# Optimization experiments

Hardware: AMD Instinct MI355X
Metric: run time of the kernel (lower is better)

## Reference

```python
import jax, jax.numpy as jnp
import numpy as np

HEADS = 16
LN_EPS = 1e-5


def setup_inputs() -> dict:
    key = jax.random.key(0)
    ks = jax.random.split(key, 4)
    B, S, C, U = 2, 2048, 1024, 1024
    scale = 1.0 / np.sqrt(C)
    return {
        "inputs": jax.random.normal(ks[0], (B, S, C), dtype=jnp.float32),
        "Wq": jax.random.normal(ks[1], (C, U), dtype=jnp.float32) * scale,
        "bq": jnp.zeros((U,), dtype=jnp.float32),
        "Wk": jax.random.normal(ks[2], (C, U), dtype=jnp.float32) * scale,
        "bk": jnp.zeros((U,), dtype=jnp.float32),
        "Wv": jax.random.normal(ks[3], (C, U), dtype=jnp.float32) * scale,
        "bv": jnp.zeros((U,), dtype=jnp.float32),
        "ln_gamma": jnp.ones((S, U), dtype=jnp.float32),
        "ln_beta": jnp.zeros((S, U), dtype=jnp.float32),
    }


def reference(inputs, Wq, bq, Wk, bk, Wv, bv, ln_gamma, ln_beta):
    B, S, C = inputs.shape
    U = Wq.shape[1]
    H = HEADS
    dh = U // H

    Q = inputs @ Wq + bq  # [B,S,U]
    K = inputs @ Wk + bk
    V = inputs @ Wv + bv

    # torch: concat(split(X, U//H, dim=-1), dim=0) -> head-major stacking on batch
    def split_heads(X):
        return jnp.moveaxis(X.reshape(B, S, H, dh), 2, 0).reshape(H * B, S, dh)

    Q_, K_, V_ = split_heads(Q), split_heads(K), split_heads(V)

    scores = jnp.einsum('bqd,bkd->bqk', Q_, K_) / jnp.sqrt(jnp.float32(dh))
    tri = jnp.tril(jnp.ones((S, S), dtype=bool))  # causal mask
    scores = jnp.where(tri[None, :, :], scores, jnp.float32(-1e9))
    attn = jax.nn.softmax(scores, axis=-1)
    out_ = jnp.einsum('bqk,bkd->bqd', attn, V_)  # [H*B,S,dh]

    # inverse: split on batch into H chunks of size B, concat on feature dim
    out = jnp.moveaxis(out_.reshape(H, B, S, dh), 0, 2).reshape(B, S, U)

    out = out + inputs  # residual

    # LayerNorm over normalized_shape=[S, U] (joint seq+feature stats)
    mu = jnp.mean(out, axis=(-2, -1), keepdims=True)
    var = jnp.mean(jnp.square(out - mu), axis=(-2, -1), keepdims=True)
    out = (out - mu) / jnp.sqrt(var + LN_EPS) * ln_gamma + ln_beta
    return out
```

## Files before the change

kernel.cpp:

```cpp
#include <hip/hip_runtime.h>
#include <hip/hip_bf16.h>


typedef __bf16 bf16_t;
typedef __bf16 bf16x8 __attribute__((ext_vector_type(8)));
typedef __bf16 bf16x4 __attribute__((ext_vector_type(4)));
typedef _Float16 f16_t;
typedef _Float16 f16x2 __attribute__((ext_vector_type(2)));
typedef _Float16 f16x4 __attribute__((ext_vector_type(4)));
typedef _Float16 f16x8 __attribute__((ext_vector_type(8)));
typedef float f32x4 __attribute__((ext_vector_type(4)));

constexpr int Bsz = 2;
constexpr int Seq = 2048;
constexpr int Cdim = 1024;
constexpr int Udim = 1024;
constexpr int Hn = 16;
constexpr int Dh = 64;
constexpr int Mrows = Bsz * Seq;
constexpr int PerBatch = Seq * Udim;
constexpr float SCLQ = 0.125f * 1.44269504088896340736f;

#if __has_builtin(__builtin_amdgcn_exp2f)
#define EXP2F(x) __builtin_amdgcn_exp2f(x)
#else
#define EXP2F(x) exp2f(x)
#endif

#define AINL __attribute__((always_inline))

__device__ __forceinline__ void gload16(const void* g, void* l)
{
    __builtin_amdgcn_global_load_lds(
        (const __attribute__((address_space(1))) void*)g,
        (__attribute__((address_space(3))) void*)l, 16, 0, 0);
}

__device__ __forceinline__ f16x2 pkrtz(float a, float b)
{
    return __builtin_bit_cast(f16x2, __builtin_amdgcn_cvt_pkrtz(a, b));
}

__global__ __launch_bounds__(256)
void prep(const float* __restrict__ X,
          const float* __restrict__ Wq, const float* __restrict__ Wk,
          const float* __restrict__ Wv,
          bf16_t* __restrict__ Xb,
          bf16_t* __restrict__ Tq, bf16_t* __restrict__ Tk,
          bf16_t* __restrict__ Tv, float* __restrict__ stats)
{
    int z = blockIdx.z;
    int tid = threadIdx.x;
    if (z < 3) {
        const float* W = (z == 0) ? Wq : (z == 1) ? Wk : Wv;
        bf16_t* T = (z == 0) ? Tq : (z == 1) ? Tk : Tv;
        __shared__ bf16_t t[64][65];
        int x0 = blockIdx.x * 64, y0 = blockIdx.y * 64;
        int tx = tid & 63, ty = tid >> 6;
        for (int i = ty; i < 64; i += 4)
            t[i][tx] = (bf16_t)W[(size_t)(y0 + i) * Cdim + x0 + tx];
        __syncthreads();
        for (int i = ty; i < 64; i += 4)
            T[(size_t)(x0 + i) * Cdim + y0 + tx] = t[tx][i];
    } else {
        int bi = blockIdx.y * 16 + blockIdx.x;
        if (bi == 0 && tid < 4) stats[tid] = 0.0f;
        const float4* Xv = (const float4*)X;
#pragma unroll
        for (int k = 0; k < 16; k++) {
            int i = bi * 4096 + k * 256 + tid;
            float4 v = Xv[i];
            bf16x4 o = { (bf16_t)v.x, (bf16_t)v.y, (bf16_t)v.z, (bf16_t)v.w };
            *(bf16x4*)(Xb + (size_t)i * 4) = o;
        }
    }
}

__global__ __launch_bounds__(256)
void gemm_qkv(const bf16_t* __restrict__ X,
              const bf16_t* __restrict__ Wt0, const bf16_t* __restrict__ Wt1,
              const bf16_t* __restrict__ Wt2,
              const float* __restrict__ b0, const float* __restrict__ b1,
              const float* __restrict__ b2,
              f16_t* __restrict__ O0, f16_t* __restrict__ O1, f16_t* __restrict__ O2v)
{
    int z = blockIdx.z;
    const bf16_t* Wt = (z == 0) ? Wt0 : (z == 1) ? Wt1 : Wt2;
    const float* bias = (z == 0) ? b0 : (z == 1) ? b1 : b2;
    float scl = (z == 0) ? SCLQ : 1.0f;

    constexpr int Kd = 1024, Nd = 1024;
    __shared__ __align__(16) bf16_t As[128 * 32];
    __shared__ __align__(16) bf16_t Bs[128 * 32];

    int tid = threadIdx.x;
    int wave = tid >> 6, lane = tid & 63, quad = lane >> 4, l16 = lane & 15;
    int wm = (wave & 1) * 64, wn = (wave >> 1) * 64;
    int m0 = blockIdx.y * 128, n0 = blockIdx.x * 128;

    f32x4 acc[4][4] = {};

    int e0 = wave * 512 + lane * 8;
    int r0 = e0 >> 5, c0 = e0 & 31;
    int e1 = e0 + 2048;
    int r1 = e1 >> 5, c1 = e1 & 31;
    const bf16_t* Ag = X + (size_t)m0 * Kd;
    const bf16_t* Bg = Wt + (size_t)n0 * Kd;
    bf16_t* AsW0 = As + wave * 512;
    bf16_t* AsW1 = As + 2048 + wave * 512;
    bf16_t* BsW0 = Bs + wave * 512;
    bf16_t* BsW1 = Bs + 2048 + wave * 512;

    for (int k0 = 0; k0 < Kd; k0 += 32) {
        gload16(Ag + (size_t)r0 * Kd + k0 + c0, AsW0);
        gload16(Ag + (size_t)r1 * Kd + k0 + c1, AsW1);
        gload16(Bg + (size_t)r0 * Kd + k0 + c0, BsW0);
        gload16(Bg + (size_t)r1 * Kd + k0 + c1, BsW1);
        __syncthreads();

        bf16x8 af[4], bfr[4];
#pragma unroll
        for (int i = 0; i < 4; i++)
            af[i] = *(const bf16x8*)&As[(wm + i * 16 + l16) * 32 + quad * 8];
#pragma unroll
        for (int i = 0; i < 4; i++)
            bfr[i] = *(const bf16x8*)&Bs[(wn + i * 16 + l16) * 32 + quad * 8];
#pragma unroll
        for (int mt = 0; mt < 4; mt++)
#pragma unroll
            for (int nt = 0; nt < 4; nt++)
                acc[mt][nt] = __builtin_amdgcn_mfma_f32_16x16x32_bf16(
                    af[mt], bfr[nt], acc[mt][nt], 0, 0, 0);
        __syncthreads();
    }

    if (z < 2) {
        f16_t* Og = (z == 0) ? O0 : O1;
#pragma unroll
        for (int nt = 0; nt < 4; nt++) {
            int col = n0 + wn + nt * 16 + l16;
            float bv = bias[col];
#pragma unroll
            for (int mt = 0; mt < 4; mt++) {
                int row = m0 + wm + mt * 16 + quad * 4;
#pragma unroll
                for (int r = 0; r < 4; r++)
                    Og[(size_t)(row + r) * Nd + col] = (f16_t)((acc[mt][nt][r] + bv) * scl);
            }
        }
    } else {
        int bb = m0 >> 11;
#pragma unroll
        for (int nt = 0; nt < 4; nt++) {
            int col = n0 + wn + nt * 16 + l16;
            float bv = bias[col];
            int h = col >> 6, d = col & 63;
            f16_t* vbase = O2v + (((size_t)(bb * Hn + h) * Dh + d) << 11);
#pragma unroll
            for (int mt = 0; mt < 4; mt++) {
                int row = m0 + wm + mt * 16 + quad * 4;
                int s = row & (Seq - 1);
                f16x4 pk;
#pragma unroll
                for (int r = 0; r < 4; r++) pk[r] = (f16_t)(acc[mt][nt][r] + bv);
                *(f16x4*)(vbase + s) = pk;
            }
        }
    }
}

__global__ __launch_bounds__(512, 4)
void attn12(const f16_t* __restrict__ Q, const f16_t* __restrict__ K,
            const f16_t* __restrict__ Vt, const float* __restrict__ X,
            bf16_t* __restrict__ R, float* __restrict__ stats)
{
    int id = blockIdx.x;
    int c = id & 7;
    int rr = id >> 3;
    int g = rr & 3;
    int pi = rr >> 2;
    int bh = (g << 3) | c;
    int b = bh >> 4, h = bh & 15;
    int qa = 31 - pi, qb = pi, split = 15 - pi;

    int tid = threadIdx.x;
    int grp = tid >> 8;
    int w = (tid >> 6) & 3;
    int lane = tid & 63, quad = lane >> 4, l16 = lane & 15;
    size_t bS = (size_t)b * Seq;

    __shared__ __align__(16) char ldsRaw[65600];
    f16_t* KsBase = (f16_t*)(ldsRaw + grp * 32768);
    f16_t* VsBase = (f16_t*)(ldsRaw + grp * 32768 + 16384);
    float* cmbO   = (float*)(ldsRaw + 32768);
    float* cmbLS  = (float*)(ldsRaw + 49152);
    float* red    = (float*)(ldsRaw + 65536);

    const f16_t* Kg = K + bS * Udim + h * Dh;
    const f16_t* Vg = Vt + ((size_t)(b * Hn + h)) * Dh * Seq;

    int srow = w * 8 + (lane >> 3);
    int schunk = (lane & 7) ^ ((lane >> 3) & 7);

    int qidxA = qa * 64 + w * 16 + l16;
    int qidxB = qb * 64 + w * 16 + l16;
    const f16_t* QpA = Q + (bS + qidxA) * Udim + h * Dh;
    const f16_t* QpB = Q + (bS + qidxB) * Udim + h * Dh;
    f16x8 qfA[2], qfB[2];
#pragma unroll
    for (int s2 = 0; s2 < 2; s2++) {
        qfA[s2] = *(const f16x8*)(QpA + s2 * 32 + quad * 8);
        qfB[s2] = *(const f16x8*)(QpB + s2 * 32 + quad * 8);
    }

    int m = l16 & 7;
    int kO0 = l16 * 64 + ((quad ^ m) << 3);
    int kO1 = l16 * 64 + (((4 + quad) ^ m) << 3);
    int vO[4];
#pragma unroll
    for (int t = 0; t < 4; t++)
        vO[t] = l16 * 64 + (((t * 32 + quad * 8) ^ (m << 4)) >> 1);

    f32x4 OA[4] = {}, OB[4] = {};
    float lsA = 0.0f, lsB = 0.0f;

    auto STAGE = [&](int nb, int tl) AINL {
        const f16_t* kp = Kg + (size_t)(tl * 64 + srow) * Udim + schunk * 8;
        const f16_t* vp = Vg + (size_t)srow * Seq + tl * 64 + schunk * 8;
        f16_t* kd = KsBase + nb * 4096;
        f16_t* vd = VsBase + nb * 4096;
        gload16(kp, kd + w * 512);
        gload16(kp + (size_t)32 * Udim, kd + 2048 + w * 512);
        gload16(vp, vd + w * 512);
        gload16(vp + (size_t)32 * Seq, vd + 2048 + w * 512);
    };

    auto CN = [&](int buf, const f16x8 (&qf)[2], f32x4 (&O)[4], float& ls) AINL {
        const f16_t* Kb = KsBase + buf * 4096;
        const f16_t* Vb = VsBase + buf * 4096;
        f32x4 st[4];
#pragma unroll
        for (int t = 0; t < 4; t++) {
            f16x8 kf0 = *(const f16x8*)&Kb[kO0 + t * 1024];
            f16x8 kf1 = *(const f16x8*)&Kb[kO1 + t * 1024];
            f32x4 a = {};
            a = __builtin_amdgcn_mfma_f32_16x16x32_f16(kf0, qf[0], a, 0, 0, 0);
            a = __builtin_amdgcn_mfma_f32_16x16x32_f16(kf1, qf[1], a, 0, 0, 0);
            st[t] = a;
        }
        f16x4 pf[4];
#pragma unroll
        for (int t = 0; t < 4; t++) {
            float p0 = EXP2F(st[t][0]);
            float p1 = EXP2F(st[t][1]);
            float p2 = EXP2F(st[t][2]);
            float p3 = EXP2F(st[t][3]);
            ls += (p0 + p1) + (p2 + p3);
            f16x2 lo = pkrtz(p0, p1);
            f16x2 hi = pkrtz(p2, p3);
            pf[t][0] = lo[0]; pf[t][1] = lo[1];
            pf[t][2] = hi[0]; pf[t][3] = hi[1];
        }
#pragma unroll
        for (int t = 0; t < 4; t++)
#pragma unroll
            for (int dt = 0; dt < 4; dt++) {
                f16x4 vf = *(const f16x4*)&Vb[vO[t] + dt * 1024];
                O[dt] = __builtin_amdgcn_mfma_f32_16x16x16f16(vf, pf[t], O[dt], 0, 0, 0);
            }
    };

    auto CM = [&](int buf, const f16x8 (&qf)[2], f32x4 (&O)[4], float& ls,
                  int kv0, int qidx) AINL {
        const f16_t* Kb = KsBase + buf * 4096;
        const f16_t* Vb = VsBase + buf * 4096;
#pragma unroll
        for (int t = 0; t < 4; t++) {
            if (t <= w) {
                f16x8 kf0 = *(const f16x8*)&Kb[kO0 + t * 1024];
                f16x8 kf1 = *(const f16x8*)&Kb[kO1 + t * 1024];
                f32x4 a = {};
                a = __builtin_amdgcn_mfma_f32_16x16x32_f16(kf0, qf[0], a, 0, 0, 0);
                a = __builtin_amdgcn_mfma_f32_16x16x32_f16(kf1, qf[1], a, 0, 0, 0);
                f16x4 pfd;
#pragma unroll
                for (int r2 = 0; r2 < 4; r2++) {
                    float sv = a[r2];
                    if (kv0 + t * 16 + quad * 4 + r2 > qidx) sv = -1e30f;
                    float pv = EXP2F(sv);
                    ls += pv;
                    pfd[r2] = (f16_t)pv;
                }
#pragma unroll
                for (int dt = 0; dt < 4; dt++) {
                    f16x4 vf = *(const f16x4*)&Vb[vO[t] + dt * 1024];
                    O[dt] = __builtin_amdgcn_mfma_f32_16x16x16f16(vf, pfd, O[dt], 0, 0, 0);
                }
            }
        }
    };

    STAGE(0, (grp == 0) ? 0 : split);
    __syncthreads();

    int r = 0;
    auto ROUND = [&](int buf) AINL {
        if (r < 16) {
            int rn = r + 1;
            int tl = (grp == 0) ? ((rn <= qb) ? rn : rn - qb - 1) : (split + rn);
            STAGE(buf ^ 1, tl);
        }
        if (grp == 0) {
            if (r < qb)       CN(buf, qfB, OB, lsB);
            else if (r == qb) CM(buf, qfB, OB, lsB, qb * 64, qidxB);
            else if (r < 16)  CN(buf, qfA, OA, lsA);
        } else {
            if (r < 16)       CN(buf, qfA, OA, lsA);
            else              CM(buf, qfA, OA, lsA, qa * 64, qidxA);
        }
        __syncthreads();
        r++;
    };

    for (int i = 0; i < 8; i++) { ROUND(0); ROUND(1); }
    ROUND(0);

    lsA += __shfl_xor(lsA, 16);
    lsA += __shfl_xor(lsA, 32);

    float s_acc = 0.0f, ss_acc = 0.0f;

    if (grp == 1) {
        float* po = cmbO + w * 1024 + lane * 16;
#pragma unroll
        for (int dt = 0; dt < 4; dt++)
            *(f32x4*)(po + dt * 4) = OA[dt];
        if (lane < 16) cmbLS[w * 16 + l16] = lsA;
    } else {
        lsB += __shfl_xor(lsB, 16);
        lsB += __shfl_xor(lsB, 32);
        float invB = 1.0f / lsB;
        const float* XpB = X + (bS + qidxB) * Udim + h * Dh;
        bf16_t* RpB = R + (bS + qidxB) * Udim + h * Dh;
#pragma unroll
        for (int dt = 0; dt < 4; dt++) {
            f32x4 xv = *(const f32x4*)(XpB + dt * 16 + quad * 4);
            f32x4 o = OB[dt] * invB + xv;
            bf16x4 ob;
#pragma unroll
            for (int r2 = 0; r2 < 4; r2++) {
                ob[r2] = (bf16_t)o[r2];
                s_acc += o[r2];
                ss_acc += o[r2] * o[r2];
            }
            *(bf16x4*)(RpB + dt * 16 + quad * 4) = ob;
        }
    }
    __syncthreads();

    if (grp == 0) {
        const float* po = cmbO + w * 1024 + lane * 16;
#pragma unroll
        for (int dt = 0; dt < 4; dt++)
            OA[dt] += *(const f32x4*)(po + dt * 4);
        lsA += cmbLS[w * 16 + l16];
        float invA = 1.0f / lsA;
        const float* XpA = X + (bS + qidxA) * Udim + h * Dh;
        bf16_t* RpA = R + (bS + qidxA) * Udim + h * Dh;
#pragma unroll
        for (int dt = 0; dt < 4; dt++) {
            f32x4 xv = *(const f32x4*)(XpA + dt * 16 + quad * 4);
            f32x4 o = OA[dt] * invA + xv;
            bf16x4 ob;
#pragma unroll
            for (int r2 = 0; r2 < 4; r2++) {
                ob[r2] = (bf16_t)o[r2];
                s_acc += o[r2];
                ss_acc += o[r2] * o[r2];
            }
            *(bf16x4*)(RpA + dt * 16 + quad * 4) = ob;
        }
    }

#pragma unroll
    for (int o = 1; o < 64; o <<= 1) {
        s_acc += __shfl_xor(s_acc, o);
        ss_acc += __shfl_xor(ss_acc, o);
    }
    int w8 = tid >> 6;
    if (lane == 0) { red[w8] = s_acc; red[8 + w8] = ss_acc; }
    __syncthreads();
    if (tid == 0) {
        float s = 0.0f, ss = 0.0f;
#pragma unroll
        for (int i = 0; i < 8; i++) { s += red[i]; ss += red[8 + i]; }
        atomicAdd(&stats[b], s);
        atomicAdd(&stats[2 + b], ss);
    }
}

__global__ __launch_bounds__(256)
void ln_norm(const bf16_t* __restrict__ R, const float* __restrict__ gamma,
             const float* __restrict__ beta, const float* __restrict__ stats,
             float* __restrict__ out)
{
    constexpr float invN = 1.0f / (float)PerBatch;
    float mu[2], inv[2];
#pragma unroll
    for (int b = 0; b < 2; b++) {
        float m = stats[b] * invN;
        float var = stats[2 + b] * invN - m * m;
        mu[b] = m;
        inv[b] = rsqrtf(var + 1e-5f);
    }
    int i = blockIdx.x * 256 + threadIdx.x;
    int f = i * 8;
    int b = f >> 21;
    int su = f & (PerBatch - 1);
    bf16x8 rv = *(const bf16x8*)(R + f);
    float4 g0 = *(const float4*)(gamma + su);
    float4 g1 = *(const float4*)(gamma + su + 4);
    float4 be0 = *(const float4*)(beta + su);
    float4 be1 = *(const float4*)(beta + su + 4);
    float4 o0, o1;
    o0.x = ((float)rv[0] - mu[b]) * inv[b] * g0.x + be0.x;
    o0.y = ((float)rv[1] - mu[b]) * inv[b] * g0.y + be0.y;
    o0.z = ((float)rv[2] - mu[b]) * inv[b] * g0.z + be0.z;
    o0.w = ((float)rv[3] - mu[b]) * inv[b] * g0.w + be0.w;
    o1.x = ((float)rv[4] - mu[b]) * inv[b] * g1.x + be1.x;
    o1.y = ((float)rv[5] - mu[b]) * inv[b] * g1.y + be1.y;
    o1.z = ((float)rv[6] - mu[b]) * inv[b] * g1.z + be1.z;
    o1.w = ((float)rv[7] - mu[b]) * inv[b] * g1.w + be1.w;
    *(float4*)(out + f) = o0;
    *(float4*)(out + f + 4) = o1;
}

extern "C" void kernel_launch(void* const* d_in, const int* in_sizes, int n_in,
                              void* d_out, int out_size, void* d_ws, size_t ws_size,
                              hipStream_t stream)
{
    const float* X     = (const float*)d_in[0];
    const float* Wq    = (const float*)d_in[1];
    const float* bq    = (const float*)d_in[2];
    const float* Wk    = (const float*)d_in[3];
    const float* bk    = (const float*)d_in[4];
    const float* Wv    = (const float*)d_in[5];
    const float* bv    = (const float*)d_in[6];
    const float* gamma = (const float*)d_in[7];
    const float* beta  = (const float*)d_in[8];
    float* out = (float*)d_out;

    char* ws = (char*)d_ws;
    size_t off = 0;
    auto alloc = [&](size_t bytes) -> void* {
        void* p = ws + off;
        off += (bytes + 255) & ~(size_t)255;
        return p;
    };
    bf16_t* Xb = (bf16_t*)alloc((size_t)Mrows * Cdim * 2);
    bf16_t* Tq = (bf16_t*)alloc((size_t)Cdim * Udim * 2);
    bf16_t* Tk = (bf16_t*)alloc((size_t)Cdim * Udim * 2);
    bf16_t* Tv = (bf16_t*)alloc((size_t)Cdim * Udim * 2);
    f16_t*  Qb = (f16_t*)alloc((size_t)Mrows * Udim * 2);
    f16_t*  Kb = (f16_t*)alloc((size_t)Mrows * Udim * 2);
    f16_t*  Vtb = (f16_t*)alloc((size_t)Mrows * Udim * 2);
    bf16_t* Rb = (bf16_t*)alloc((size_t)Mrows * Udim * 2);
    float*  stats = (float*)alloc(4 * sizeof(float));

    prep<<<dim3(16, 16, 4), 256, 0, stream>>>(X, Wq, Wk, Wv, Xb, Tq, Tk, Tv, stats);
    gemm_qkv<<<dim3(8, 32, 3), 256, 0, stream>>>(Xb, Tq, Tk, Tv, bq, bk, bv, Qb, Kb, Vtb);
    attn12<<<dim3(512), 512, 0, stream>>>(Qb, Kb, Vtb, X, Rb, stats);
    ln_norm<<<dim3(2048), 256, 0, stream>>>(Rb, gamma, beta, stats, out);
}
```

Before: 185.1 us.

## Double-buffer QKV GEMM loads and use manual vmcnt waits in attention

The QKV GEMM now keeps two LDS buffers and prefetches the next K-slice with global_load_lds while computing on the current one. Explicit s_barrier plus s_waitcnt vmcnt(4) replaces the full __syncthreads drain, so only the older loads must land before compute. The attention kernel gets the same restructuring: its prefetch loop uses partial vmcnt waits and sched barriers instead of a trailing __syncthreads. The point is to overlap global-to-LDS traffic with MFMA work, at the cost of twice the GEMM LDS and correctness that depends on the hand-counted vmcnt values.

```diff
diff --git a/kernel.cpp b/kernel.cpp
--- a/kernel.cpp
+++ b/kernel.cpp
@@ -28,6 +28,10 @@
 #endif
 
 #define AINL __attribute__((always_inline))
+#define BARRIER() __builtin_amdgcn_s_barrier()
+#define SCHEDB() __builtin_amdgcn_sched_barrier(0)
+#define WAITV4() asm volatile("s_waitcnt vmcnt(4)" ::: "memory")
+#define WAITV0() asm volatile("s_waitcnt vmcnt(0)" ::: "memory")
 
 __device__ __forceinline__ void gload16(const void* g, void* l)
 {
@@ -90,8 +94,8 @@
     float scl = (z == 0) ? SCLQ : 1.0f;
 
     constexpr int Kd = 1024, Nd = 1024;
-    __shared__ __align__(16) bf16_t As[128 * 32];
-    __shared__ __align__(16) bf16_t Bs[128 * 32];
+    __shared__ __align__(16) bf16_t As[2][4096];
+    __shared__ __align__(16) bf16_t Bs[2][4096];
 
     int tid = threadIdx.x;
     int wave = tid >> 6, lane = tid & 63, quad = lane >> 4, l16 = lane & 15;
@@ -106,33 +110,40 @@
     int r1 = e1 >> 5, c1 = e1 & 31;
     const bf16_t* Ag = X + (size_t)m0 * Kd;
     const bf16_t* Bg = Wt + (size_t)n0 * Kd;
-    bf16_t* AsW0 = As + wave * 512;
-    bf16_t* AsW1 = As + 2048 + wave * 512;
-    bf16_t* BsW0 = Bs + wave * 512;
-    bf16_t* BsW1 = Bs + 2048 + wave * 512;
-
-    for (int k0 = 0; k0 < Kd; k0 += 32) {
-        gload16(Ag + (size_t)r0 * Kd + k0 + c0, AsW0);
-        gload16(Ag + (size_t)r1 * Kd + k0 + c1, AsW1);
-        gload16(Bg + (size_t)r0 * Kd + k0 + c0, BsW0);
-        gload16(Bg + (size_t)r1 * Kd + k0 + c1, BsW1);
-        __syncthreads();
-
+
+    auto STG = [&](int nb, int k0) AINL {
+        gload16(Ag + (size_t)r0 * Kd + k0 + c0, &As[nb][wave * 512]);
+        gload16(Ag + (size_t)r1 * Kd + k0 + c1, &As[nb][2048 + wave * 512]);
+        gload16(Bg + (size_t)r0 * Kd + k0 + c0, &Bs[nb][wave * 512]);
+        gload16(Bg + (size_t)r1 * Kd + k0 + c1, &Bs[nb][2048 + wave * 512]);
+    };
+
+    int kNext = 32;
+    auto STEP = [&](int buf, bool doStage) AINL {
+        BARRIER();
+        if (doStage) { STG(buf ^ 1, kNext); kNext += 32; WAITV4(); }
+        else WAITV0();
+        BARRIER();
+        SCHEDB();
         bf16x8 af[4], bfr[4];
 #pragma unroll
         for (int i = 0; i < 4; i++)
-            af[i] = *(const bf16x8*)&As[(wm + i * 16 + l16) * 32 + quad * 8];
+            af[i] = *(const bf16x8*)&As[buf][(wm + i * 16 + l16) * 32 + quad * 8];
 #pragma unroll
         for (int i = 0; i < 4; i++)
-            bfr[i] = *(const bf16x8*)&Bs[(wn + i * 16 + l16) * 32 + quad * 8];
+            bfr[i] = *(const bf16x8*)&Bs[buf][(wn + i * 16 + l16) * 32 + quad * 8];
 #pragma unroll
         for (int mt = 0; mt < 4; mt++)
 #pragma unroll
             for (int nt = 0; nt < 4; nt++)
                 acc[mt][nt] = __builtin_amdgcn_mfma_f32_16x16x32_bf16(
                     af[mt], bfr[nt], acc[mt][nt], 0, 0, 0);
-        __syncthreads();
-    }
+    };
+
+    STG(0, 0);
+    for (int it = 0; it < 15; it++) { STEP(0, true); STEP(1, true); }
+    STEP(0, true);
+    STEP(1, false);
 
     if (z < 2) {
         f16_t* Og = (z == 0) ? O0 : O1;
@@ -170,7 +181,7 @@
 }
 
 __global__ __launch_bounds__(512, 4)
-void attn12(const f16_t* __restrict__ Q, const f16_t* __restrict__ K,
+void attn13(const f16_t* __restrict__ Q, const f16_t* __restrict__ K,
             const f16_t* __restrict__ Vt, const float* __restrict__ X,
             bf16_t* __restrict__ R, float* __restrict__ stats)
 {
@@ -300,16 +311,19 @@
         }
     };
 
-    STAGE(0, (grp == 0) ? 0 : split);
-    __syncthreads();
-
     int r = 0;
     auto ROUND = [&](int buf) AINL {
+        BARRIER();
         if (r < 16) {
             int rn = r + 1;
             int tl = (grp == 0) ? ((rn <= qb) ? rn : rn - qb - 1) : (split + rn);
             STAGE(buf ^ 1, tl);
-        }
+            WAITV4();
+        } else {
+            WAITV0();
+        }
+        BARRIER();
+        SCHEDB();
         if (grp == 0) {
             if (r < qb)       CN(buf, qfB, OB, lsB);
             else if (r == qb) CM(buf, qfB, OB, lsB, qb * 64, qidxB);
@@ -318,12 +332,14 @@
             if (r < 16)       CN(buf, qfA, OA, lsA);
             else              CM(buf, qfA, OA, lsA, qa * 64, qidxA);
         }
-        __syncthreads();
         r++;
     };
 
+    STAGE(0, (grp == 0) ? 0 : split);
     for (int i = 0; i < 8; i++) { ROUND(0); ROUND(1); }
     ROUND(0);
+
+    BARRIER();
 
     lsA += __shfl_xor(lsA, 16);
     lsA += __shfl_xor(lsA, 32);
@@ -469,6 +485,6 @@
 
     prep<<<dim3(16, 16, 4), 256, 0, stream>>>(X, Wq, Wk, Wv, Xb, Tq, Tk, Tv, stats);
     gemm_qkv<<<dim3(8, 32, 3), 256, 0, stream>>>(Xb, Tq, Tk, Tv, bq, bk, bv, Qb, Kb, Vtb);
-    attn12<<<dim3(512), 512, 0, stream>>>(Qb, Kb, Vtb, X, Rb, stats);
+    attn13<<<dim3(512), 512, 0, stream>>>(Qb, Kb, Vtb, X, Rb, stats);
     ln_norm<<<dim3(2048), 256, 0, stream>>>(Rb, gamma, beta, stats, out);
 }
```

New measurement: 184.0 us. Within noise of the previous version (-0.6%).
